# Performance work log

Hardware: AMD Instinct MI355X
Metric: run time of the kernel (lower is better)

Reference implementation:

```python
import jax, jax.numpy as jnp
import numpy as np

B, S, IN_DIM, MEM, LAYERS, HEADS, TOP_K = 64, 256, 512, 256, 3, 8, 200


def setup_inputs() -> dict:
    key = jax.random.key(0)
    ks = jax.random.split(key, 16)
    inputs = jax.random.normal(ks[0], (B, S, IN_DIM), jnp.float32)
    # dependency-style sparse 0/1 adjacency, symmetric with self loops
    a = (jax.random.uniform(ks[1], (B, S, S)) < 0.05).astype(jnp.float32)
    adj = jnp.clip(a + jnp.swapaxes(a, -1, -2) + jnp.eye(S, dtype=jnp.float32), 0.0, 1.0)
    lengths = jnp.maximum(jax.random.randint(ks[2], (B,), 0, S + 1), 32)
    pad = jnp.arange(S)[None, :] >= lengths[:, None]  # [B,S] True at pad positions
    score_mask = pad[:, None, :, None] | pad[:, None, None, :]  # [B,1,S,S]
    d = {"adj": adj, "inputs": inputs, "score_mask": score_mask}

    def lin(k, din, dout):
        k1, k2 = jax.random.split(k)
        s = 1.0 / np.sqrt(din)
        return (jax.random.uniform(k1, (din, dout), jnp.float32, -s, s),
                jax.random.uniform(k2, (dout,), jnp.float32, -s, s))

    ki = 3
    for l in range(LAYERS):
        w, b = lin(ks[ki], IN_DIM + l * MEM, MEM); ki += 1
        d[f"W{l}_w"], d[f"W{l}_b"] = w, b
    for i in range(LAYERS - 1):
        din = IN_DIM + (i + 1) * MEM
        qw, qb = lin(ks[ki], din, din); ki += 1
        kw, kb = lin(ks[ki], din, din); ki += 1
        d[f"attn{i}_qw"], d[f"attn{i}_qb"] = qw, qb
        d[f"attn{i}_kw"], d[f"attn{i}_kb"] = kw, kb
    return d


def _gcn_layer(adj, x, denom, W, b):
    # AxW = W(adj @ x) / denom ; out = relu(AxW) + W(x)   (dropout=identity, eval)
    AxW = ((adj @ x) @ W + b) / denom
    return jax.nn.relu(AxW) + (x @ W + b)


def _mha_adj(x, qw, qb, kw, kb, mask):
    Bn, Sn, D = x.shape
    dk = D // HEADS
    q = (x @ qw + qb).reshape(Bn, Sn, HEADS, dk).transpose(0, 2, 1, 3)
    k = (x @ kw + kb).reshape(Bn, Sn, HEADS, dk).transpose(0, 2, 1, 3)
    scores = jnp.einsum('bhqd,bhkd->bhqk', q, k) / jnp.sqrt(jnp.float32(dk))
    scores = jnp.where(mask, jnp.float32(-1e9), scores)
    keep = (~mask[:, :, :, 0:1]).astype(scores.dtype)  # zero out pad query rows
    return jax.nn.softmax(scores, axis=-1) * keep


def _select(m, top_num):
    # per-batch top-k threshold over flattened [S*S], symmetrize, diag := 1
    Bn, Sn, _ = m.shape
    flat = m.reshape(Bn, -1)
    thr = jax.lax.top_k(flat, top_num)[0][:, -1:]
    sel = (flat >= thr).astype(m.dtype).reshape(Bn, Sn, Sn)
    sel = sel + jnp.swapaxes(sel, -1, -2)
    eye = jnp.eye(Sn, dtype=m.dtype)
    return sel * (1.0 - eye) + eye


def reference(adj, inputs, score_mask, W0_w, W0_b, W1_w, W1_b, W2_w, W2_b,
              attn0_qw, attn0_qb, attn0_kw, attn0_kb,
              attn1_qw, attn1_qb, attn1_kw, attn1_kb):
    Ws = [(W0_w, W0_b), (W1_w, W1_b), (W2_w, W2_b)]
    attns = [(attn0_qw, attn0_qb, attn0_kw, attn0_kb),
             (attn1_qw, attn1_qb, attn1_kw, attn1_kb)]
    denom = adj.sum(2, keepdims=True) + 1.0
    out = _gcn_layer(adj, inputs, denom, *Ws[0])
    x = inputs
    for i in range(1, LAYERS):
        x = jnp.concatenate([x, out], axis=-1)  # growing concatenated features
        a = _mha_adj(x, *attns[i - 1], score_mask)  # [B,H,S,S]
        a = a.sum(axis=1)  # second_layer='sum' branch
        a = _select(a, TOP_K) * a
        denom = a.sum(2, keepdims=True) + 1.0
        out = _gcn_layer(a, x, denom, *Ws[i])
    return out
```

## Files before the change

### kernel.cpp

```cpp
#include <hip/hip_runtime.h>
#include <math.h>


typedef __attribute__((ext_vector_type(8))) short s16x8;
typedef __attribute__((ext_vector_type(4))) float f32x4;

__device__ __forceinline__ short f2bf(float x) {
    unsigned u = __float_as_uint(x);
    u += 0x7FFF + ((u >> 16) & 1);
    return (short)(u >> 16);
}
__device__ __forceinline__ float bf2f(short h) {
    return __uint_as_float(((unsigned)(unsigned short)h) << 16);
}

__device__ __forceinline__ void gl2l(const void* g, void* l) {
    __builtin_amdgcn_global_load_lds(
        (const __attribute__((address_space(1))) unsigned int*)g,
        (__attribute__((address_space(3))) unsigned int*)l, 16, 0, 0);
}

__global__ void init_flags(int* flags) {
    if (threadIdx.x < 3) flags[threadIdx.x] = 0;
}

__global__ void detect_mask(const unsigned int* __restrict__ w, int nwords, int* flags) {
    int stride = gridDim.x * blockDim.x;
    int l_u8 = 0, l_f32 = 0, l_nz = 0;
    for (int i = blockIdx.x * blockDim.x + threadIdx.x; i < nwords; i += stride) {
        unsigned v = w[i];
        if (v) {
            l_nz = 1;
            if (v == 0x3F800000u) l_f32 = 1;
            else if (v > 1u) l_u8 = 1;
        }
    }
    if (__ballot(l_u8) && (threadIdx.x & 63) == 0) atomicOr(&flags[0], 1);
    if (__ballot(l_f32) && (threadIdx.x & 63) == 0) atomicOr(&flags[1], 1);
    if (__ballot(l_nz) && (threadIdx.x & 63) == 0) atomicOr(&flags[2], 1);
}

__global__ void extract_pad(const void* __restrict__ mask, const int* __restrict__ flags,
                            unsigned char* __restrict__ pad) {
    int b = blockIdx.x, i = threadIdx.x;
    int v;
    size_t idx = (size_t)b * 65536 + (size_t)i * 256;
    if (flags[0]) v = ((const unsigned char*)mask)[idx] != 0;
    else if (flags[2]) v = ((const unsigned int*)mask)[idx] != 0;
    else v = 0;
    pad[b * 256 + i] = (unsigned char)v;
}

__global__ void split_mat(const float* __restrict__ src, int ldsrc, int width,
                          short* __restrict__ dh, short* __restrict__ dl, int ldd) {
    int row = blockIdx.x;
    for (int c = threadIdx.x; c < width; c += 256) {
        float v = src[(size_t)row * ldsrc + c];
        short h = f2bf(v);
        dh[(size_t)row * ldd + c] = h;
        dl[(size_t)row * ldd + c] = f2bf(v - bf2f(h));
    }
}

__global__ void transpose_split(const float* __restrict__ in,
                                short* __restrict__ outh, short* __restrict__ outl,
                                int R, int C, int HR, long PSTR, int rowoff, int outld) {
    __shared__ float tile[32][33];
    int c0 = blockIdx.x * 32, r0 = blockIdx.y * 32;
    int tx = threadIdx.x & 31, ty = threadIdx.x >> 5;
    for (int rr = ty; rr < 32; rr += 8)
        tile[rr][tx] = in[(size_t)(r0 + rr) * C + c0 + tx];
    __syncthreads();
    for (int rr = ty; rr < 32; rr += 8) {
        float v = tile[tx][rr];
        int orow = c0 + rr;
        size_t o = (size_t)(orow / HR) * PSTR + (size_t)((orow % HR) + rowoff) * outld + (r0 + tx);
        short h = f2bf(v);
        outh[o] = h;
        outl[o] = f2bf(v - bf2f(h));
    }
}

__global__ void pack_bias2(const float* __restrict__ qb, const float* __restrict__ kb,
                           float* __restrict__ dst, int D) {
    int i = blockIdx.x * 256 + threadIdx.x;
    if (i < D) {
        int p = i / (D / 2), r = i % (D / 2);
        dst[(size_t)p * D + r] = qb[i];
        dst[(size_t)p * D + D / 2 + r] = kb[i];
    }
}

__global__ __launch_bounds__(256) void mgemm(
    const short* __restrict__ Ah, const short* __restrict__ Al,
    const short* __restrict__ Bh, const short* __restrict__ Bl,
    const float* __restrict__ bias,
    float* __restrict__ C, short* __restrict__ Ch, short* __restrict__ Cl,
    const unsigned char* __restrict__ padArr,
    int K, int lda, int ldb, int ldc) {
    int m0 = blockIdx.x * 128, n0 = blockIdx.y * 128;
    if (padArr && padArr[m0]) return;
    __shared__ short lds[16384];
    int t = threadIdx.x;
    int lane = t & 63, w = t >> 6;
    int wm = w >> 1, wn = w & 1;
    f32x4 acc[4][4];
#pragma unroll
    for (int i = 0; i < 4; ++i)
#pragma unroll
        for (int j = 0; j < 4; ++j)
            acc[i][j] = (f32x4){0.f, 0.f, 0.f, 0.f};

    for (int k0 = 0; k0 < K; k0 += 32) {
        __syncthreads();
#pragma unroll
        for (int p = 0; p < 2; ++p) {
            int s = t + p * 256;
            int mi = (s >> 6) * 16 + (s & 15);
            int koff = k0 + ((s >> 4) & 3) * 8;
            size_t oa = (size_t)(m0 + mi) * lda + koff;
            size_t ob = (size_t)(n0 + mi) * ldb + koff;
            gl2l(Ah + oa, &lds[s * 8]);
            gl2l(Al + oa, &lds[4096 + s * 8]);
            gl2l(Bh + ob, &lds[8192 + s * 8]);
            gl2l(Bl + ob, &lds[12288 + s * 8]);
        }
        __syncthreads();
        s16x8 ah[4], al4[4], bh[4], bl4[4];
#pragma unroll
        for (int i = 0; i < 4; ++i) {
            int off = ((wm * 4 + i) * 64 + lane) * 8;
            ah[i] = *(const s16x8*)&lds[off];
            al4[i] = *(const s16x8*)&lds[4096 + off];
        }
#pragma unroll
        for (int j = 0; j < 4; ++j) {
            int off = ((wn * 4 + j) * 64 + lane) * 8;
            bh[j] = *(const s16x8*)&lds[8192 + off];
            bl4[j] = *(const s16x8*)&lds[12288 + off];
        }
#pragma unroll
        for (int i = 0; i < 4; ++i)
#pragma unroll
            for (int j = 0; j < 4; ++j) {
                acc[i][j] = __builtin_amdgcn_mfma_f32_16x16x32_bf16(ah[i], bh[j], acc[i][j], 0, 0, 0);
                acc[i][j] = __builtin_amdgcn_mfma_f32_16x16x32_bf16(ah[i], bl4[j], acc[i][j], 0, 0, 0);
                acc[i][j] = __builtin_amdgcn_mfma_f32_16x16x32_bf16(al4[i], bh[j], acc[i][j], 0, 0, 0);
            }
    }

    int col = lane & 15, quad = lane >> 4;
#pragma unroll
    for (int i = 0; i < 4; ++i)
#pragma unroll
        for (int j = 0; j < 4; ++j) {
            int mg = m0 + wm * 64 + i * 16 + quad * 4;
            int ng = n0 + wn * 64 + j * 16 + col;
            f32x4 v = acc[i][j];
            float bz = bias ? bias[ng] : 0.f;
            float o[4];
#pragma unroll
            for (int r = 0; r < 4; ++r) o[r] = v[r] + bz;
            if (C) {
#pragma unroll
                for (int r = 0; r < 4; ++r)
                    C[(size_t)(mg + r) * ldc + ng] = o[r];
            } else {
#pragma unroll
                for (int r = 0; r < 4; ++r) {
                    short hh = f2bf(o[r]);
                    Ch[(size_t)(mg + r) * ldc + ng] = hh;
                    Cl[(size_t)(mg + r) * ldc + ng] = f2bf(o[r] - bf2f(hh));
                }
            }
        }
}

__global__ void spmm_gcn(const float* __restrict__ A, const float* __restrict__ tz,
                         const float* __restrict__ bias,
                         short* __restrict__ oh, short* __restrict__ ol,
                         float* __restrict__ of, int ldo, int coloff) {
    int row = blockIdx.x * 4 + (threadIdx.x >> 6);
    int lane = threadIdx.x & 63;
    int b = row >> 8;
    float4 av = ((const float4*)(A + (size_t)row * 256))[lane];
    const float* tzb = tz + (size_t)(b << 8) * 256;
    float4 acc = make_float4(0.f, 0.f, 0.f, 0.f);
    float rs = av.x + av.y + av.z + av.w;
#pragma unroll
    for (int o = 32; o; o >>= 1) rs += __shfl_xor(rs, o);
    for (int s = 0; s < 64; ++s) {
        float vx = __shfl(av.x, s), vy = __shfl(av.y, s);
        float vz = __shfl(av.z, s), vw = __shfl(av.w, s);
        const float* tj = tzb + (size_t)(s << 2) * 256;
        if (vx != 0.f) {
            float4 tv = ((const float4*)tj)[lane];
            acc.x += vx * tv.x; acc.y += vx * tv.y; acc.z += vx * tv.z; acc.w += vx * tv.w;
        }
        if (vy != 0.f) {
            float4 tv = ((const float4*)(tj + 256))[lane];
            acc.x += vy * tv.x; acc.y += vy * tv.y; acc.z += vy * tv.z; acc.w += vy * tv.w;
        }
        if (vz != 0.f) {
            float4 tv = ((const float4*)(tj + 512))[lane];
            acc.x += vz * tv.x; acc.y += vz * tv.y; acc.z += vz * tv.z; acc.w += vz * tv.w;
        }
        if (vw != 0.f) {
            float4 tv = ((const float4*)(tj + 768))[lane];
            acc.x += vw * tv.x; acc.y += vw * tv.y; acc.z += vw * tv.z; acc.w += vw * tv.w;
        }
    }
    float inv = 1.f / (rs + 1.f);
    float4 b4 = ((const float4*)bias)[lane];
    float4 t4 = ((const float4*)(tz + (size_t)row * 256))[lane];
    float4 o;
    o.x = fmaxf((acc.x + b4.x) * inv, 0.f) + t4.x + b4.x;
    o.y = fmaxf((acc.y + b4.y) * inv, 0.f) + t4.y + b4.y;
    o.z = fmaxf((acc.z + b4.z) * inv, 0.f) + t4.z + b4.z;
    o.w = fmaxf((acc.w + b4.w) * inv, 0.f) + t4.w + b4.w;
    if (of) {
        ((float4*)(of + (size_t)row * ldo))[lane] = o;
    } else {
        size_t base = (size_t)row * ldo + coloff + lane * 4;
        float vv[4] = {o.x, o.y, o.z, o.w};
#pragma unroll
        for (int r = 0; r < 4; ++r) {
            short hh = f2bf(vv[r]);
            oh[base + r] = hh;
            ol[base + r] = f2bf(vv[r] - bf2f(hh));
        }
    }
}

__global__ __launch_bounds__(256) void attn_fused(
    const short* __restrict__ QKh, const short* __restrict__ QKl,
    const unsigned char* __restrict__ pad, float* __restrict__ a4,
    int D, int dk, float scale) {
    int HD = D / 2;
    int b = blockIdx.y;
    int m0 = blockIdx.x * 64;
    const unsigned char* pb = pad + (b << 8);
    if (pb[m0]) return;
    int t = threadIdx.x, lane = t & 63, w = t >> 6;
    int wm = w >> 1, wn = w & 1;
    int col16 = lane & 15, quad = lane >> 4;
    __shared__ short lds[20480];
    __shared__ float redm[64][2];
    __shared__ float reds[64][2];
    unsigned cmask = 0;
#pragma unroll
    for (int j = 0; j < 8; ++j)
        if (pb[wn * 128 + j * 16 + col16]) cmask |= 1u << j;
    float* a4b = a4 + (size_t)blockIdx.z * 4194304;
    size_t rowQ = (size_t)(b << 8) + m0;
    size_t rowK = (size_t)(b << 8);
    float aacc[2][8][4];
#pragma unroll
    for (int i = 0; i < 2; ++i)
#pragma unroll
        for (int j = 0; j < 8; ++j)
#pragma unroll
            for (int r = 0; r < 4; ++r) aacc[i][j][r] = 0.f;

    for (int hh = 0; hh < 2; ++hh) {
        int hs = blockIdx.z * 2 + hh;
        int qo = hs * dk, ko = HD + hs * dk;
        f32x4 acc[2][8];
#pragma unroll
        for (int i = 0; i < 2; ++i)
#pragma unroll
            for (int j = 0; j < 8; ++j) acc[i][j] = (f32x4){0.f, 0.f, 0.f, 0.f};
        for (int k0 = 0; k0 < dk; k0 += 32) {
            __syncthreads();
            {
                int mi = ((t >> 6) << 4) + (t & 15);
                int kc = ((t >> 4) & 3) << 3;
                size_t o = (rowQ + mi) * D + qo + k0 + kc;
                gl2l(QKh + o, &lds[t * 8]);
                gl2l(QKl + o, &lds[2048 + t * 8]);
            }
#pragma unroll
            for (int kk = 0; kk < 4; ++kk) {
                int s = t + (kk << 8);
                int ni = ((s >> 6) << 4) + (s & 15);
                int kc = ((s >> 4) & 3) << 3;
                size_t o = (rowK + ni) * D + ko + k0 + kc;
                gl2l(QKh + o, &lds[4096 + s * 8]);
                gl2l(QKl + o, &lds[12288 + s * 8]);
            }
            __syncthreads();
            s16x8 qh[2], ql[2];
#pragma unroll
            for (int i = 0; i < 2; ++i) {
                int off = ((wm * 2 + i) * 64 + lane) * 8;
                qh[i] = *(const s16x8*)&lds[off];
                ql[i] = *(const s16x8*)&lds[2048 + off];
            }
#pragma unroll
            for (int j = 0; j < 8; ++j) {
                int off = ((wn * 8 + j) * 64 + lane) * 8;
                s16x8 kh = *(const s16x8*)&lds[4096 + off];
                s16x8 kl = *(const s16x8*)&lds[12288 + off];
#pragma unroll
                for (int i = 0; i < 2; ++i) {
                    acc[i][j] = __builtin_amdgcn_mfma_f32_16x16x32_bf16(qh[i], kh, acc[i][j], 0, 0, 0);
                    acc[i][j] = __builtin_amdgcn_mfma_f32_16x16x32_bf16(qh[i], kl, acc[i][j], 0, 0, 0);
                    acc[i][j] = __builtin_amdgcn_mfma_f32_16x16x32_bf16(ql[i], kh, acc[i][j], 0, 0, 0);
                }
            }
        }
        float rmax[2][4];
#pragma unroll
        for (int i = 0; i < 2; ++i)
#pragma unroll
            for (int r = 0; r < 4; ++r) rmax[i][r] = -1e30f;
#pragma unroll
        for (int i = 0; i < 2; ++i)
#pragma unroll
            for (int j = 0; j < 8; ++j) {
                bool msk = (cmask >> j) & 1;
#pragma unroll
                for (int r = 0; r < 4; ++r) {
                    float v = msk ? -1e30f : acc[i][j][r] * scale;
                    acc[i][j][r] = v;
                    rmax[i][r] = fmaxf(rmax[i][r], v);
                }
            }
#pragma unroll
        for (int ms = 1; ms < 16; ms <<= 1)
#pragma unroll
            for (int i = 0; i < 2; ++i)
#pragma unroll
                for (int r = 0; r < 4; ++r)
                    rmax[i][r] = fmaxf(rmax[i][r], __shfl_xor(rmax[i][r], ms));
        if (col16 == 0)
#pragma unroll
            for (int i = 0; i < 2; ++i)
#pragma unroll
                for (int r = 0; r < 4; ++r)
                    redm[wm * 32 + i * 16 + quad * 4 + r][wn] = rmax[i][r];
        __syncthreads();
#pragma unroll
        for (int i = 0; i < 2; ++i)
#pragma unroll
            for (int r = 0; r < 4; ++r) {
                int rr = wm * 32 + i * 16 + quad * 4 + r;
                rmax[i][r] = fmaxf(redm[rr][0], redm[rr][1]);
            }
        float rsum[2][4];
#pragma unroll
        for (int i = 0; i < 2; ++i)
#pragma unroll
            for (int r = 0; r < 4; ++r) rsum[i][r] = 0.f;
#pragma unroll
        for (int i = 0; i < 2; ++i)
#pragma unroll
            for (int j = 0; j < 8; ++j) {
                bool msk = (cmask >> j) & 1;
#pragma unroll
                for (int r = 0; r < 4; ++r) {
                    float p = msk ? 0.f : __expf(acc[i][j][r] - rmax[i][r]);
                    acc[i][j][r] = p;
                    rsum[i][r] += p;
                }
            }
#pragma unroll
        for (int ms = 1; ms < 16; ms <<= 1)
#pragma unroll
            for (int i = 0; i < 2; ++i)
#pragma unroll
                for (int r = 0; r < 4; ++r)
                    rsum[i][r] += __shfl_xor(rsum[i][r], ms);
        if (col16 == 0)
#pragma unroll
            for (int i = 0; i < 2; ++i)
#pragma unroll
                for (int r = 0; r < 4; ++r)
                    reds[wm * 32 + i * 16 + quad * 4 + r][wn] = rsum[i][r];
        __syncthreads();
#pragma unroll
        for (int i = 0; i < 2; ++i)
#pragma unroll
            for (int r = 0; r < 4; ++r) {
                int rr = wm * 32 + i * 16 + quad * 4 + r;
                float tot = reds[rr][0] + reds[rr][1];
                float inv = tot > 0.f ? 1.f / tot : 0.f;
#pragma unroll
                for (int j = 0; j < 8; ++j)
                    aacc[i][j][r] += acc[i][j][r] * inv;
            }
    }
#pragma unroll
    for (int i = 0; i < 2; ++i)
#pragma unroll
        for (int r = 0; r < 4; ++r) {
            size_t rb = (rowQ + wm * 32 + i * 16 + quad * 4 + r) * 256;
#pragma unroll
            for (int j = 0; j < 8; ++j)
                a4b[rb + wn * 128 + j * 16 + col16] = aacc[i][j][r];
        }
}

__global__ void add4(const float* __restrict__ a4, const unsigned char* __restrict__ pad,
                     float* __restrict__ a) {
    int row = blockIdx.x * 4 + (threadIdx.x >> 6);
    int lane = threadIdx.x & 63;
    size_t o = (size_t)row * 256 + lane * 4;
    float4 s = make_float4(0.f, 0.f, 0.f, 0.f);
    if (!pad[row]) {
#pragma unroll
        for (int z = 0; z < 4; ++z) {
            float4 v = *(const float4*)(a4 + (size_t)z * 4194304 + o);
            s.x += v.x; s.y += v.y; s.z += v.z; s.w += v.w;
        }
    }
    *(float4*)(a + o) = s;
}

__global__ void tk_init(unsigned* ghist, unsigned* prefix, int* krem) {
    int i = blockIdx.x * 256 + threadIdx.x;
    ghist[i] = 0;
    if (i < 64) { prefix[i] = 0; krem[i] = 200; }
}

__global__ void tk_hist(const float* __restrict__ a, const unsigned* __restrict__ prefix,
                        unsigned* __restrict__ ghist, int shift) {
    __shared__ unsigned h[256];
    int b = blockIdx.x >> 4, slice = blockIdx.x & 15;
    h[threadIdx.x] = 0;
    __syncthreads();
    unsigned pfx = prefix[b];
    const unsigned* ab = (const unsigned*)(a + (size_t)b * 65536) + slice * 4096;
    for (int i = threadIdx.x; i < 4096; i += 256) {
        unsigned u = ab[i];
        if ((shift == 24) || ((u >> (shift + 8)) == pfx)) atomicAdd(&h[(u >> shift) & 255], 1u);
    }
    __syncthreads();
    if (h[threadIdx.x]) atomicAdd(&ghist[b * 256 + threadIdx.x], h[threadIdx.x]);
}

__global__ void tk_pick(unsigned* __restrict__ ghist, unsigned* __restrict__ prefix,
                        int* __restrict__ krem, float* __restrict__ thr, int last) {
    __shared__ unsigned h[256];
    int b = blockIdx.x;
    h[threadIdx.x] = ghist[b * 256 + threadIdx.x];
    ghist[b * 256 + threadIdx.x] = 0;
    __syncthreads();
    if (!threadIdx.x) {
        int k = krem[b];
        unsigned c = 0;
        int bin = 255;
        for (; bin >= 0; --bin) { c += h[bin]; if ((int)c >= k) break; }
        if (bin < 0) bin = 0;
        krem[b] = k - (int)(c - h[bin]);
        unsigned p = (prefix[b] << 8) | (unsigned)bin;
        prefix[b] = p;
        if (last) thr[b] = __uint_as_float(p);
    }
}

__global__ void select_apply(const float* __restrict__ a, const float* __restrict__ thr,
                             float* __restrict__ a2) {
    int row = blockIdx.x;
    int b = row >> 8, i = row & 255, j = threadIdx.x;
    const float* ab = a + (size_t)b * 65536;
    float tb = thr[b];
    float v = ab[i * 256 + j];
    float vt = ab[j * 256 + i];
    float sel = (v >= tb ? 1.f : 0.f) + (vt >= tb ? 1.f : 0.f);
    if (i == j) sel = 1.f;
    a2[(size_t)row * 256 + j] = v * sel;
}

extern "C" void kernel_launch(void* const* d_in, const int* in_sizes, int n_in,
                              void* d_out, int out_size, void* d_ws, size_t ws_size,
                              hipStream_t stream) {
    const float* adj = (const float*)d_in[0];
    const float* x0 = (const float*)d_in[1];
    const void* mask = d_in[2];
    const float* Wls[3] = {(const float*)d_in[3], (const float*)d_in[5], (const float*)d_in[7]};
    const float* bls[3] = {(const float*)d_in[4], (const float*)d_in[6], (const float*)d_in[8]};
    const float* qws[2] = {(const float*)d_in[9], (const float*)d_in[13]};
    const float* qbs[2] = {(const float*)d_in[10], (const float*)d_in[14]};
    const float* kws[2] = {(const float*)d_in[11], (const float*)d_in[15]};
    const float* kbs[2] = {(const float*)d_in[12], (const float*)d_in[16]};

    char* base = (char*)d_ws;
    size_t cur = 0;
    auto alloc = [&](size_t bytes) -> void* {
        cur = (cur + 1023) & ~(size_t)1023;
        void* p = base + cur;
        cur += bytes;
        return p;
    };
    const size_t NROW = 16384;
    const size_t SEG = NROW * 256;
    int* flags = (int*)alloc(12);
    unsigned char* pad = (unsigned char*)alloc(NROW);
    float* thr = (float*)alloc(256);
    unsigned* prefix = (unsigned*)alloc(256);
    int* krem = (int*)alloc(256);
    unsigned* ghist = (unsigned*)alloc(64 * 256 * 4);
    short* WTh = (short*)alloc((size_t)2304 * 256 * 2);
    short* WTl = (short*)alloc((size_t)2304 * 256 * 2);
    short* qkwPh = (short*)alloc((size_t)2 * 1024 * 1024 * 2);
    short* qkwPl = (short*)alloc((size_t)2 * 1024 * 1024 * 2);
    float* qkb = (float*)alloc((size_t)2 * 1024 * 4);
    short* xh = (short*)alloc(NROW * 1024 * 2);
    short* xl = (short*)alloc(NROW * 1024 * 2);
    float* a4 = (float*)alloc(4 * SEG * 4);
    short* QKh = (short*)alloc(NROW * 1024 * 2);
    short* QKl = (short*)alloc(NROW * 1024 * 2);
    if (ws_size < cur) return;

    float* a = a4;
    float* tzf = a4 + SEG;
    float* a2f = a4 + 3 * SEG;
    const int Ks[3] = {512, 768, 1024};
    const long offW[3] = {0, (long)512 * 256, (long)(512 + 768) * 256};

    init_flags<<<1, 64, 0, stream>>>(flags);
    detect_mask<<<64, 256, 0, stream>>>((const unsigned int*)mask, 1048576, flags);
    extract_pad<<<64, 256, 0, stream>>>(mask, flags, pad);
    split_mat<<<16384, 256, 0, stream>>>(x0, 512, 512, xh, xl, 1024);
    for (int l = 0; l < 3; ++l)
        transpose_split<<<dim3(8, Ks[l] / 32), 256, 0, stream>>>(
            Wls[l], WTh + offW[l], WTl + offW[l], Ks[l], 256, 256, 0, 0, Ks[l]);

    for (int l = 0; l < 3; ++l) {
        int Kl = Ks[l];
        mgemm<<<dim3(128, 2, 1), 256, 0, stream>>>(
            xh, xl, WTh + offW[l], WTl + offW[l], nullptr,
            tzf, nullptr, nullptr, nullptr, Kl, 1024, Kl, 256);
        const float* Aadj = (l == 0) ? adj : a2f;
        if (l < 2) {
            spmm_gcn<<<4096, 256, 0, stream>>>(
                Aadj, tzf, bls[l], xh, xl, nullptr, 1024, Kl);
        } else {
            spmm_gcn<<<4096, 256, 0, stream>>>(
                Aadj, tzf, bls[l], nullptr, nullptr, (float*)d_out, 256, 0);
            break;
        }

        int D = Ks[l + 1], dk = D / 8, HD = D / 2;
        float scale = 1.f / sqrtf((float)dk);
        transpose_split<<<dim3(D / 32, D / 32), 256, 0, stream>>>(
            qws[l], qkwPh, qkwPl, D, D, HD, (long)D * D, 0, D);
        transpose_split<<<dim3(D / 32, D / 32), 256, 0, stream>>>(
            kws[l], qkwPh, qkwPl, D, D, HD, (long)D * D, HD, D);
        pack_bias2<<<4, 256, 0, stream>>>(qbs[l], kbs[l], qkb, D);

        for (int p = 0; p < 2; ++p) {
            mgemm<<<dim3(128, D / 128, 1), 256, 0, stream>>>(
                xh, xl, qkwPh + (size_t)p * D * D, qkwPl + (size_t)p * D * D,
                qkb + (size_t)p * D, nullptr, QKh, QKl, pad, D, 1024, D, D);
            attn_fused<<<dim3(4, 64, 2), 256, 0, stream>>>(
                QKh, QKl, pad, a4 + (size_t)p * 2 * SEG, D, dk, scale);
        }
        add4<<<4096, 256, 0, stream>>>(a4, pad, a);
        tk_init<<<64, 256, 0, stream>>>(ghist, prefix, krem);
        for (int pp = 0; pp < 4; ++pp) {
            tk_hist<<<1024, 256, 0, stream>>>(a, prefix, ghist, 24 - 8 * pp);
            tk_pick<<<64, 256, 0, stream>>>(ghist, prefix, krem, thr, pp == 3);
        }
        select_apply<<<16384, 256, 0, stream>>>(a, thr, a2f);
    }
}
```

Measured before the change: 1.384 ms.

## Fuse GCN weight GEMM into QK projection and accumulate attention sums in place

For layers one and two, the x@W GEMM is appended as extra output columns of the first Q/K projection GEMM, so it runs in the same launch and writes fp32 to a separate buffer. That GEMM also skips pad rows except for those extra columns. The second attention pass now adds into the first pass's output instead of writing new buffers, so add4 becomes add2 with half the reads. The GEMM block index is swizzled across M tiles, which may change cache locality. Workspace shrinks, but the accumulate path adds a read-modify-write in attention.

```diff
diff --git a/kernel.cpp b/kernel.cpp
--- a/kernel.cpp
+++ b/kernel.cpp
@@ -84,11 +84,13 @@
 __global__ void pack_bias2(const float* __restrict__ qb, const float* __restrict__ kb,
                            float* __restrict__ dst, int D) {
     int i = blockIdx.x * 256 + threadIdx.x;
+    int HD = D / 2, PS = D + 256;
     if (i < D) {
-        int p = i / (D / 2), r = i % (D / 2);
-        dst[(size_t)p * D + r] = qb[i];
-        dst[(size_t)p * D + D / 2 + r] = kb[i];
-    }
+        int p = i / HD, r = i % HD;
+        dst[(size_t)p * PS + r] = qb[i];
+        dst[(size_t)p * PS + HD + r] = kb[i];
+    }
+    if (i < 256) dst[D + i] = 0.f;
 }
 
 __global__ __launch_bounds__(256) void mgemm(
@@ -96,10 +98,12 @@
     const short* __restrict__ Bh, const short* __restrict__ Bl,
     const float* __restrict__ bias,
     float* __restrict__ C, short* __restrict__ Ch, short* __restrict__ Cl,
-    const unsigned char* __restrict__ padArr,
-    int K, int lda, int ldb, int ldc) {
-    int m0 = blockIdx.x * 128, n0 = blockIdx.y * 128;
-    if (padArr && padArr[m0]) return;
+    float* __restrict__ Ct, const unsigned char* __restrict__ padArr,
+    int K, int lda, int ldb, int ldc, int nsplit) {
+    int mt = (blockIdx.x + 8 * blockIdx.y) & 127;
+    int m0 = mt * 128, n0 = blockIdx.y * 128;
+    bool isTz = (Ct != nullptr) && (n0 >= nsplit);
+    if (padArr && padArr[m0] && !isTz) return;
     __shared__ short lds[16384];
     int t = threadIdx.x;
     int lane = t & 63, w = t >> 6;
@@ -161,7 +165,11 @@
             float o[4];
 #pragma unroll
             for (int r = 0; r < 4; ++r) o[r] = v[r] + bz;
-            if (C) {
+            if (isTz) {
+#pragma unroll
+                for (int r = 0; r < 4; ++r)
+                    Ct[(size_t)(mg + r) * 256 + (ng - nsplit)] = o[r];
+            } else if (C) {
 #pragma unroll
                 for (int r = 0; r < 4; ++r)
                     C[(size_t)(mg + r) * ldc + ng] = o[r];
@@ -235,7 +243,7 @@
 __global__ __launch_bounds__(256) void attn_fused(
     const short* __restrict__ QKh, const short* __restrict__ QKl,
     const unsigned char* __restrict__ pad, float* __restrict__ a4,
-    int D, int dk, float scale) {
+    int D, int dk, float scale, int accum) {
     int HD = D / 2;
     int b = blockIdx.y;
     int m0 = blockIdx.x * 64;
@@ -396,23 +404,25 @@
         for (int r = 0; r < 4; ++r) {
             size_t rb = (rowQ + wm * 32 + i * 16 + quad * 4 + r) * 256;
 #pragma unroll
-            for (int j = 0; j < 8; ++j)
-                a4b[rb + wn * 128 + j * 16 + col16] = aacc[i][j][r];
-        }
-}
-
-__global__ void add4(const float* __restrict__ a4, const unsigned char* __restrict__ pad,
+            for (int j = 0; j < 8; ++j) {
+                size_t o = rb + wn * 128 + j * 16 + col16;
+                float v = aacc[i][j][r];
+                if (accum) v += a4b[o];
+                a4b[o] = v;
+            }
+        }
+}
+
+__global__ void add2(const float* __restrict__ a4, const unsigned char* __restrict__ pad,
                      float* __restrict__ a) {
     int row = blockIdx.x * 4 + (threadIdx.x >> 6);
     int lane = threadIdx.x & 63;
     size_t o = (size_t)row * 256 + lane * 4;
     float4 s = make_float4(0.f, 0.f, 0.f, 0.f);
     if (!pad[row]) {
-#pragma unroll
-        for (int z = 0; z < 4; ++z) {
-            float4 v = *(const float4*)(a4 + (size_t)z * 4194304 + o);
-            s.x += v.x; s.y += v.y; s.z += v.z; s.w += v.w;
-        }
+        float4 v0 = *(const float4*)(a4 + o);
+        float4 v1 = *(const float4*)(a4 + 4194304 + o);
+        s.x = v0.x + v1.x; s.y = v0.y + v1.y; s.z = v0.z + v1.z; s.w = v0.w + v1.w;
     }
     *(float4*)(a + o) = s;
 }
@@ -501,63 +511,65 @@
     unsigned* prefix = (unsigned*)alloc(256);
     int* krem = (int*)alloc(256);
     unsigned* ghist = (unsigned*)alloc(64 * 256 * 4);
-    short* WTh = (short*)alloc((size_t)2304 * 256 * 2);
-    short* WTl = (short*)alloc((size_t)2304 * 256 * 2);
-    short* qkwPh = (short*)alloc((size_t)2 * 1024 * 1024 * 2);
-    short* qkwPl = (short*)alloc((size_t)2 * 1024 * 1024 * 2);
-    float* qkb = (float*)alloc((size_t)2 * 1024 * 4);
+    short* WTh = (short*)alloc((size_t)256 * 512 * 2);
+    short* WTl = (short*)alloc((size_t)256 * 512 * 2);
+    short* qkwPh = (short*)alloc((size_t)2 * 1280 * 1024 * 2);
+    short* qkwPl = (short*)alloc((size_t)2 * 1280 * 1024 * 2);
+    float* qkb = (float*)alloc((size_t)2 * 1280 * 4);
     short* xh = (short*)alloc(NROW * 1024 * 2);
     short* xl = (short*)alloc(NROW * 1024 * 2);
-    float* a4 = (float*)alloc(4 * SEG * 4);
+    float* tzf = (float*)alloc(SEG * 4);
+    float* a4 = (float*)alloc(2 * SEG * 4);
     short* QKh = (short*)alloc(NROW * 1024 * 2);
     short* QKl = (short*)alloc(NROW * 1024 * 2);
     if (ws_size < cur) return;
 
     float* a = a4;
-    float* tzf = a4 + SEG;
-    float* a2f = a4 + 3 * SEG;
+    float* a2f = a4 + SEG;
     const int Ks[3] = {512, 768, 1024};
-    const long offW[3] = {0, (long)512 * 256, (long)(512 + 768) * 256};
 
     init_flags<<<1, 64, 0, stream>>>(flags);
     detect_mask<<<64, 256, 0, stream>>>((const unsigned int*)mask, 1048576, flags);
     extract_pad<<<64, 256, 0, stream>>>(mask, flags, pad);
     split_mat<<<16384, 256, 0, stream>>>(x0, 512, 512, xh, xl, 1024);
-    for (int l = 0; l < 3; ++l)
-        transpose_split<<<dim3(8, Ks[l] / 32), 256, 0, stream>>>(
-            Wls[l], WTh + offW[l], WTl + offW[l], Ks[l], 256, 256, 0, 0, Ks[l]);
+    transpose_split<<<dim3(8, 16), 256, 0, stream>>>(Wls[0], WTh, WTl, 512, 256, 256, 0, 0, 512);
 
     for (int l = 0; l < 3; ++l) {
-        int Kl = Ks[l];
-        mgemm<<<dim3(128, 2, 1), 256, 0, stream>>>(
-            xh, xl, WTh + offW[l], WTl + offW[l], nullptr,
-            tzf, nullptr, nullptr, nullptr, Kl, 1024, Kl, 256);
+        if (l == 0) {
+            mgemm<<<dim3(128, 2), 256, 0, stream>>>(
+                xh, xl, WTh, WTl, nullptr,
+                tzf, nullptr, nullptr, nullptr, nullptr, 512, 1024, 512, 256, 0);
+        }
         const float* Aadj = (l == 0) ? adj : a2f;
         if (l < 2) {
             spmm_gcn<<<4096, 256, 0, stream>>>(
-                Aadj, tzf, bls[l], xh, xl, nullptr, 1024, Kl);
+                Aadj, tzf, bls[l], xh, xl, nullptr, 1024, Ks[l]);
         } else {
             spmm_gcn<<<4096, 256, 0, stream>>>(
                 Aadj, tzf, bls[l], nullptr, nullptr, (float*)d_out, 256, 0);
             break;
         }
 
-        int D = Ks[l + 1], dk = D / 8, HD = D / 2;
+        int D = Ks[l + 1], dk = D / 8, HD = D / 2, PS = D + 256;
         float scale = 1.f / sqrtf((float)dk);
         transpose_split<<<dim3(D / 32, D / 32), 256, 0, stream>>>(
-            qws[l], qkwPh, qkwPl, D, D, HD, (long)D * D, 0, D);
+            qws[l], qkwPh, qkwPl, D, D, HD, (long)PS * D, 0, D);
         transpose_split<<<dim3(D / 32, D / 32), 256, 0, stream>>>(
-            kws[l], qkwPh, qkwPl, D, D, HD, (long)D * D, HD, D);
+            kws[l], qkwPh, qkwPl, D, D, HD, (long)PS * D, HD, D);
+        transpose_split<<<dim3(8, D / 32), 256, 0, stream>>>(
+            Wls[l + 1], qkwPh, qkwPl, D, 256, 256, 0, D, D);
         pack_bias2<<<4, 256, 0, stream>>>(qbs[l], kbs[l], qkb, D);
 
-        for (int p = 0; p < 2; ++p) {
-            mgemm<<<dim3(128, D / 128, 1), 256, 0, stream>>>(
-                xh, xl, qkwPh + (size_t)p * D * D, qkwPl + (size_t)p * D * D,
-                qkb + (size_t)p * D, nullptr, QKh, QKl, pad, D, 1024, D, D);
-            attn_fused<<<dim3(4, 64, 2), 256, 0, stream>>>(
-                QKh, QKl, pad, a4 + (size_t)p * 2 * SEG, D, dk, scale);
-        }
-        add4<<<4096, 256, 0, stream>>>(a4, pad, a);
+        mgemm<<<dim3(128, PS / 128), 256, 0, stream>>>(
+            xh, xl, qkwPh, qkwPl, qkb,
+            nullptr, QKh, QKl, tzf, pad, D, 1024, D, D, D);
+        attn_fused<<<dim3(4, 64, 2), 256, 0, stream>>>(QKh, QKl, pad, a4, D, dk, scale, 0);
+        mgemm<<<dim3(128, D / 128), 256, 0, stream>>>(
+            xh, xl, qkwPh + (size_t)PS * D, qkwPl + (size_t)PS * D, qkb + PS,
+            nullptr, QKh, QKl, nullptr, pad, D, 1024, D, D, D);
+        attn_fused<<<dim3(4, 64, 2), 256, 0, stream>>>(QKh, QKl, pad, a4, D, dk, scale, 1);
+
+        add2<<<4096, 256, 0, stream>>>(a4, pad, a);
         tk_init<<<64, 256, 0, stream>>>(ghist, prefix, krem);
         for (int pp = 0; pp < 4; ++pp) {
             tk_hist<<<1024, 256, 0, stream>>>(a, prefix, ghist, 24 - 8 * pp);
```

Measured after the change: 1.390 ms. About the same (+0.4%).
